# Kernel tuning notes

Hardware: AMD Instinct MI355X
Metric: run time of the kernel (lower is better)

## Reference

```python
import jax, jax.numpy as jnp
import numpy as np

N_NODES = 50000
N_EDGES = 800000
IN_FEAT = 128
INTER_DIM = 128
OUT_FEAT = 128
EDGE_W_DIM = 3


def setup_inputs() -> dict:
    key = jax.random.key(0)
    ks = jax.random.split(key, 8)
    h = jax.random.normal(ks[0], (N_NODES, IN_FEAT), dtype=jnp.float32)
    edge_src = jax.random.randint(ks[1], (N_EDGES,), 0, N_NODES, dtype=jnp.int32)
    edge_dst = jax.random.randint(ks[2], (N_EDGES,), 0, N_NODES, dtype=jnp.int32)
    edge_w = jax.random.normal(ks[3], (N_EDGES, EDGE_W_DIM), dtype=jnp.float32)
    # xavier-normal-ish init, gain for relu
    gain = float(np.sqrt(2.0))
    W1 = jax.random.normal(ks[4], (INTER_DIM, IN_FEAT + EDGE_W_DIM), dtype=jnp.float32)
    W1 = W1 * (gain * np.sqrt(2.0 / (INTER_DIM + IN_FEAT + EDGE_W_DIM)))
    b1 = jnp.zeros((INTER_DIM,), dtype=jnp.float32)
    W2 = jax.random.normal(ks[5], (OUT_FEAT, IN_FEAT + INTER_DIM), dtype=jnp.float32)
    W2 = W2 * (gain * np.sqrt(2.0 / (OUT_FEAT + IN_FEAT + INTER_DIM)))
    b2 = jnp.zeros((OUT_FEAT,), dtype=jnp.float32)
    return {"h": h, "edge_src": edge_src, "edge_dst": edge_dst, "edge_w": edge_w,
            "W1": W1, "b1": b1, "W2": W2, "b2": b2}


def reference(h, edge_src, edge_dst, edge_w, W1, b1, W2, b2):
    n_nodes = h.shape[0]
    # per-edge message: concat(src node feature, edge weight) -> [E, in_feat+3]
    m = jnp.concatenate([h[edge_src], edge_w], axis=1)
    # linear1 + leaky_relu (torch default negative_slope=0.01)
    tmp = m @ W1.T + b1  # [E, inter_dim]
    tmp = jnp.where(tmp >= 0, tmp, 0.01 * tmp)
    # mean over incoming edges per destination node; zero-in-degree nodes get 0
    sums = jax.ops.segment_sum(tmp, edge_dst, num_segments=n_nodes)
    counts = jax.ops.segment_sum(jnp.ones((tmp.shape[0],), dtype=tmp.dtype),
                                 edge_dst, num_segments=n_nodes)
    h_N = sums / jnp.maximum(counts, 1.0)[:, None]  # [N, inter_dim]
    # tail: concat + linear2 + relu
    h_total = jnp.concatenate([h, h_N], axis=1)  # [N, in_feat+inter_dim]
    return jax.nn.relu(h_total @ W2.T + b2)
```

## Files before the change

kernel.cpp:

```cpp
#include <hip/hip_runtime.h>
#include <hip/hip_bf16.h>

#define N_NODES 50000
#define N_EDGES 800000
#define N_TILES 3125
#define CSR_BLOCKS 782
#define PROJ_BLOCKS 782
#define BUCKET_CAP 64

typedef __attribute__((ext_vector_type(8))) short short8;
typedef __attribute__((ext_vector_type(4))) float f32x4;
typedef __attribute__((ext_vector_type(2))) float fl2;

#define OFF_G     0
#define OFF_CUR   1600000
#define OFF_HN    6400000
#define OFF_W1BP  12866384
#define OFF_BP1   12866896
#define OFF_BP2   12875088


__device__ inline unsigned bf16rne(float f) {
    unsigned u = __float_as_uint(f);
    return (u + 0x7fffu + ((u >> 16) & 1u)) >> 16;
}
__device__ inline unsigned pk2(float lo, float hi) {
    return bf16rne(lo) | (bf16rne(hi) << 16);
}
union FragU { unsigned u[4]; short8 s; uint4 v; };

template <bool HI>
__device__ inline fl2 fp8x2_dec_w(unsigned s) {
#if __has_builtin(__builtin_amdgcn_cvt_pk_f32_fp8)
    return __builtin_amdgcn_cvt_pk_f32_fp8((int)s, HI);
#else
    unsigned v = HI ? (s >> 16) : s;
    fl2 r;
    unsigned lo = v & 0xffu, h2 = (v >> 8) & 0xffu;
    unsigned blo = ((lo & 0x80u) << 24) | ((lo & 0x7fu) << 20);
    unsigned bhi = ((h2 & 0x80u) << 24) | ((h2 & 0x7fu) << 20);
    r.x = __uint_as_float(blo) * 0x1p120f;
    r.y = __uint_as_float(bhi) * 0x1p120f;
    return r;
#endif
}
__device__ inline unsigned fp8x4_enc(float a, float b, float c, float d) {
#if __has_builtin(__builtin_amdgcn_cvt_pk_fp8_f32)
    int u = __builtin_amdgcn_cvt_pk_fp8_f32(a, b, 0, false);
    u = __builtin_amdgcn_cvt_pk_fp8_f32(c, d, u, true);
    return (unsigned)u;
#else
    auto enc1 = [](float f) -> unsigned {
        unsigned u = __float_as_uint(f);
        unsigned sg = (u >> 24) & 0x80u;
        float af = fabsf(f);
        if (af < 0x1p-6f) return sg;
        if (af >= 448.f) return sg | 0x7eu;
        unsigned v = __float_as_uint(af);
        unsigned r = v + 0xFFFFFu + ((v >> 20) & 1u);
        unsigned E = r >> 23, m = (r >> 20) & 7u;
        return sg | ((E - 120u) << 3) | m;
    };
    return enc1(a) | (enc1(b) << 8) | (enc1(c) << 16) | (enc1(d) << 24);
#endif
}

__global__ __launch_bounds__(256) void repack_zero_kernel(
        const float* __restrict__ W1, const float* __restrict__ b1,
        const float* __restrict__ W2, float* __restrict__ W1bp,
        uint4* __restrict__ Bpack1, uint4* __restrict__ Bpack2,
        int* __restrict__ cursor) {
    int tid = blockIdx.x * 256 + threadIdx.x;
    if (tid < 2048) {
        int lane = tid & 63, ent = tid >> 6;
        int n = (ent & 7) * 16 + (lane & 15);
        int k0 = (ent >> 3) * 32 + ((lane >> 4) << 3);
        const float* src = W1 + n * 131 + k0;
        FragU f;
        f.u[0] = pk2(src[0], src[1]);
        f.u[1] = pk2(src[2], src[3]);
        f.u[2] = pk2(src[4], src[5]);
        f.u[3] = pk2(src[6], src[7]);
        Bpack1[ent * 64 + lane] = f.v;
    } else if (tid < 6144) {
        int t2 = tid - 2048;
        int lane = t2 & 63, ent = t2 >> 6;
        int n = (ent & 7) * 16 + (lane & 15);
        int k0 = (ent >> 3) * 32 + ((lane >> 4) << 3);
        const float* src = W2 + n * 256 + k0;
        FragU f;
        f.u[0] = pk2(src[0], src[1]);
        f.u[1] = pk2(src[2], src[3]);
        f.u[2] = pk2(src[4], src[5]);
        f.u[3] = pk2(src[6], src[7]);
        Bpack2[ent * 64 + lane] = f.v;
    }
    if (tid < 128) {
        W1bp[tid * 4 + 0] = W1[tid * 131 + 128];
        W1bp[tid * 4 + 1] = W1[tid * 131 + 129];
        W1bp[tid * 4 + 2] = W1[tid * 131 + 130];
        W1bp[tid * 4 + 3] = b1[tid];
    }
    if (tid < N_NODES) cursor[tid] = 0;
}

__global__ __launch_bounds__(256) void fused_bucket_proj(
        const int* __restrict__ esrc, const int* __restrict__ edst,
        const float* __restrict__ ew, int* __restrict__ cursor,
        uint2* __restrict__ bkt,
        const float* __restrict__ h, const uint4* __restrict__ Bpack1,
        unsigned* __restrict__ g8) {
    __shared__ float lds[64][132];
    const int role = blockIdx.x & 1;
    const int gb = blockIdx.x >> 1;

    if (role == 0) {
        const int base = gb * 1024 + threadIdx.x;
        int dst[4], src[4];
        float w0[4], w1[4], w2[4];
        bool ok[4];
        #pragma unroll
        for (int j = 0; j < 4; j++) {
            int e = base + j * 256;
            ok[j] = e < N_EDGES;
            int ce = ok[j] ? e : 0;
            dst[j] = edst[ce];
            src[j] = esrc[ce];
            w0[j] = ew[ce * 3 + 0];
            w1[j] = ew[ce * 3 + 1];
            w2[j] = ew[ce * 3 + 2];
        }
        int pos[4];
        #pragma unroll
        for (int j = 0; j < 4; j++)
            pos[j] = ok[j] ? atomicAdd(&cursor[dst[j]], 1) : BUCKET_CAP;
        #pragma unroll
        for (int j = 0; j < 4; j++) {
            if (ok[j] && pos[j] < BUCKET_CAP) {
                uint2 rec;
                rec.x = (unsigned)src[j] | (bf16rne(w0[j]) << 16);
                rec.y = bf16rne(w1[j]) | (bf16rne(w2[j]) << 16);
                bkt[(dst[j] << 6) + pos[j]] = rec;
            }
        }
        return;
    }

    const int wave = threadIdx.x >> 6;
    const int lane = threadIdx.x & 63;
    const int T = gb * 4 + wave;

    if (T < N_TILES) {
        f32x4 acc[8];
        #pragma unroll
        for (int i = 0; i < 8; i++) acc[i] = (f32x4)(0.f);

        const int row = T * 16 + (lane & 15);
        const float* hrow = h + row * 128 + ((lane >> 4) << 3);

        #pragma unroll
        for (int kt = 0; kt < 4; kt++) {
            float4 x0 = *(const float4*)(hrow + kt * 32);
            float4 x1 = *(const float4*)(hrow + kt * 32 + 4);
            FragU a;
            a.u[0] = pk2(x0.x, x0.y);
            a.u[1] = pk2(x0.z, x0.w);
            a.u[2] = pk2(x1.x, x1.y);
            a.u[3] = pk2(x1.z, x1.w);
            #pragma unroll
            for (int nt = 0; nt < 8; nt++) {
                FragU b;
                b.v = Bpack1[(kt * 8 + nt) * 64 + lane];
                acc[nt] = __builtin_amdgcn_mfma_f32_16x16x32_bf16(a.s, b.s, acc[nt], 0, 0, 0);
            }
        }
        #pragma unroll
        for (int nt = 0; nt < 8; nt++) {
            #pragma unroll
            for (int reg = 0; reg < 4; reg++) {
                int r = ((lane >> 4) << 2) + reg;
                lds[wave * 16 + r][nt * 16 + (lane & 15)] = acc[nt][reg];
            }
        }
    }
    __syncthreads();

    const int t = threadIdx.x;
    const int nodeL = t >> 2, seg = t & 3;
    const int gnode = gb * 64 + nodeL;
    if (gnode < N_NODES) {
        #pragma unroll
        for (int i = 0; i < 2; i++) {
            const float* p = &lds[nodeL][seg * 32 + i * 16];
            uint4 o;
            o.x = fp8x4_enc(p[0],  p[1],  p[2],  p[3]);
            o.y = fp8x4_enc(p[4],  p[5],  p[6],  p[7]);
            o.z = fp8x4_enc(p[8],  p[9],  p[10], p[11]);
            o.w = fp8x4_enc(p[12], p[13], p[14], p[15]);
            ((uint4*)g8)[gnode * 8 + seg * 2 + i] = o;
        }
    }
}

#define AGG_P 4
__global__ __launch_bounds__(256) void agg_kernel(const unsigned* __restrict__ g8u,
                                                  const uint2* __restrict__ bkt,
                                                  const int* __restrict__ cursor,
                                                  const float* __restrict__ W1bp,
                                                  float* __restrict__ hN) {
    const int wave = threadIdx.x >> 6;
    const int lane = threadIdx.x & 63;
    const int half = lane >> 5;
    const int c = lane & 31;
    const int v = blockIdx.x * 4 + wave;
    if (v >= N_NODES) return;

    const int degT = cursor[v];
    const int deg = (degT < BUCKET_CAP) ? degT : BUCKET_CAP;
    const int beg = v << 6;
    const int end = beg + deg;

    const float4 w0 = ((const float4*)W1bp)[4 * c + 0];
    const float4 w1 = ((const float4*)W1bp)[4 * c + 1];
    const float4 w2 = ((const float4*)W1bp)[4 * c + 2];
    const float4 w3 = ((const float4*)W1bp)[4 * c + 3];
    const fl2 cx0 = {w0.x, w1.x}, cx1 = {w2.x, w3.x};
    const fl2 cy0 = {w0.y, w1.y}, cy1 = {w2.y, w3.y};
    const fl2 cz0 = {w0.z, w1.z}, cz1 = {w2.z, w3.z};
    const fl2 cb0 = {w0.w, w1.w}, cb1 = {w2.w, w3.w};
    const fl2 kP = (fl2)(0.505f);
    const fl2 kA = (fl2)(0.495f);

    fl2 acc0 = (fl2)(0.f), acc1 = (fl2)(0.f);

    int i = beg;
    for (; i + 2 * AGG_P <= end; i += 2 * AGG_P) {
        uint2 r[AGG_P];
        #pragma unroll
        for (int u = 0; u < AGG_P; u++) r[u] = bkt[i + 2 * u + half];
        unsigned gv[AGG_P];
        #pragma unroll
        for (int u = 0; u < AGG_P; u++) gv[u] = g8u[(r[u].x & 0xffffu) * 32 + c];
        #pragma unroll
        for (int u = 0; u < AGG_P; u++) {
            fl2 ry = (fl2)(__uint_as_float(r[u].x & 0xffff0000u));
            fl2 rz = (fl2)(__uint_as_float(r[u].y << 16));
            fl2 rw = (fl2)(__uint_as_float(r[u].y & 0xffff0000u));
            fl2 t0 = fp8x2_dec_w<false>(gv[u]) + cb0;
            t0 = __builtin_elementwise_fma(cx0, ry, t0);
            t0 = __builtin_elementwise_fma(cy0, rz, t0);
            t0 = __builtin_elementwise_fma(cz0, rw, t0);
            acc0 = __builtin_elementwise_fma(kP, t0, acc0);
            acc0 = __builtin_elementwise_fma(kA, __builtin_elementwise_abs(t0), acc0);
            fl2 t1 = fp8x2_dec_w<true>(gv[u]) + cb1;
            t1 = __builtin_elementwise_fma(cx1, ry, t1);
            t1 = __builtin_elementwise_fma(cy1, rz, t1);
            t1 = __builtin_elementwise_fma(cz1, rw, t1);
            acc1 = __builtin_elementwise_fma(kP, t1, acc1);
            acc1 = __builtin_elementwise_fma(kA, __builtin_elementwise_abs(t1), acc1);
        }
    }
    for (; i + 2 <= end; i += 2) {
        uint2 r = bkt[i + half];
        unsigned gv = g8u[(r.x & 0xffffu) * 32 + c];
        fl2 ry = (fl2)(__uint_as_float(r.x & 0xffff0000u));
        fl2 rz = (fl2)(__uint_as_float(r.y << 16));
        fl2 rw = (fl2)(__uint_as_float(r.y & 0xffff0000u));
        fl2 t0 = fp8x2_dec_w<false>(gv) + cb0;
        t0 = __builtin_elementwise_fma(cx0, ry, t0);
        t0 = __builtin_elementwise_fma(cy0, rz, t0);
        t0 = __builtin_elementwise_fma(cz0, rw, t0);
        acc0 = __builtin_elementwise_fma(kP, t0, acc0);
        acc0 = __builtin_elementwise_fma(kA, __builtin_elementwise_abs(t0), acc0);
        fl2 t1 = fp8x2_dec_w<true>(gv) + cb1;
        t1 = __builtin_elementwise_fma(cx1, ry, t1);
        t1 = __builtin_elementwise_fma(cy1, rz, t1);
        t1 = __builtin_elementwise_fma(cz1, rw, t1);
        acc1 = __builtin_elementwise_fma(kP, t1, acc1);
        acc1 = __builtin_elementwise_fma(kA, __builtin_elementwise_abs(t1), acc1);
    }
    if (i < end) {
        float sc = (half == 0) ? 1.f : 0.f;
        fl2 sP = (fl2)(0.505f * sc), sA = (fl2)(0.495f * sc);
        uint2 r = bkt[i];
        unsigned gv = g8u[(r.x & 0xffffu) * 32 + c];
        fl2 ry = (fl2)(__uint_as_float(r.x & 0xffff0000u));
        fl2 rz = (fl2)(__uint_as_float(r.y << 16));
        fl2 rw = (fl2)(__uint_as_float(r.y & 0xffff0000u));
        fl2 t0 = fp8x2_dec_w<false>(gv) + cb0;
        t0 = __builtin_elementwise_fma(cx0, ry, t0);
        t0 = __builtin_elementwise_fma(cy0, rz, t0);
        t0 = __builtin_elementwise_fma(cz0, rw, t0);
        acc0 = __builtin_elementwise_fma(sP, t0, acc0);
        acc0 = __builtin_elementwise_fma(sA, __builtin_elementwise_abs(t0), acc0);
        fl2 t1 = fp8x2_dec_w<true>(gv) + cb1;
        t1 = __builtin_elementwise_fma(cx1, ry, t1);
        t1 = __builtin_elementwise_fma(cy1, rz, t1);
        t1 = __builtin_elementwise_fma(cz1, rw, t1);
        acc1 = __builtin_elementwise_fma(sP, t1, acc1);
        acc1 = __builtin_elementwise_fma(sA, __builtin_elementwise_abs(t1), acc1);
    }

    acc0.x += __shfl_xor(acc0.x, 32);
    acc0.y += __shfl_xor(acc0.y, 32);
    acc1.x += __shfl_xor(acc1.x, 32);
    acc1.y += __shfl_xor(acc1.y, 32);
    if (half == 0) {
        float inv = 1.0f / (float)((degT > 0) ? degT : 1);
        float4 o;
        o.x = acc0.x * inv;
        o.y = acc0.y * inv;
        o.z = acc1.x * inv;
        o.w = acc1.y * inv;
        ((float4*)hN)[v * 32 + c] = o;
    }
}

__global__ __launch_bounds__(256) void final_mfma(const float* __restrict__ h,
                                                  const float* __restrict__ hN,
                                                  const uint4* __restrict__ Bpack2,
                                                  const float* __restrict__ b2,
                                                  float* __restrict__ out) {
    const int wave = threadIdx.x >> 6;
    const int lane = threadIdx.x & 63;
    const int T = blockIdx.x * 4 + wave;
    if (T >= N_TILES) return;

    f32x4 acc[8];
    #pragma unroll
    for (int i = 0; i < 8; i++) acc[i] = (f32x4)(0.f);

    const int row = T * 16 + (lane & 15);
    const int koff = (lane >> 4) << 3;
    const float* hrow = h + row * 128 + koff;
    const float* nrow = hN + row * 128 + koff;

    #pragma unroll
    for (int kt = 0; kt < 8; kt++) {
        const float* src = (kt < 4) ? (hrow + kt * 32) : (nrow + (kt - 4) * 32);
        float4 x0 = *(const float4*)(src);
        float4 x1 = *(const float4*)(src + 4);
        FragU a;
        a.u[0] = pk2(x0.x, x0.y);
        a.u[1] = pk2(x0.z, x0.w);
        a.u[2] = pk2(x1.x, x1.y);
        a.u[3] = pk2(x1.z, x1.w);
        #pragma unroll
        for (int nt = 0; nt < 8; nt++) {
            FragU b;
            b.v = Bpack2[(kt * 8 + nt) * 64 + lane];
            acc[nt] = __builtin_amdgcn_mfma_f32_16x16x32_bf16(a.s, b.s, acc[nt], 0, 0, 0);
        }
    }
    #pragma unroll
    for (int nt = 0; nt < 8; nt++) {
        int ch = nt * 16 + (lane & 15);
        float bias = b2[ch];
        #pragma unroll
        for (int reg = 0; reg < 4; reg++) {
            int node = T * 16 + ((lane >> 4) << 2) + reg;
            out[node * 128 + ch] = fmaxf(acc[nt][reg] + bias, 0.f);
        }
    }
}

extern "C" void kernel_launch(void* const* d_in, const int* in_sizes, int n_in,
                              void* d_out, int out_size, void* d_ws, size_t ws_size,
                              hipStream_t stream) {
    const float* h    = (const float*)d_in[0];
    const int*   esrc = (const int*)d_in[1];
    const int*   edst = (const int*)d_in[2];
    const float* ew   = (const float*)d_in[3];
    const float* W1   = (const float*)d_in[4];
    const float* b1   = (const float*)d_in[5];
    const float* W2   = (const float*)d_in[6];
    const float* b2   = (const float*)d_in[7];
    float* out = (float*)d_out;
    float* ws  = (float*)d_ws;

    unsigned* g8  = (unsigned*)(ws + OFF_G);
    int* cursor   = (int*)(ws + OFF_CUR);
    float* hN     = ws + OFF_HN;
    float* W1bp   = ws + OFF_W1BP;
    uint4* Bpack1 = (uint4*)(ws + OFF_BP1);
    uint4* Bpack2 = (uint4*)(ws + OFF_BP2);

    uint2* bkt = (uint2*)d_out;

    repack_zero_kernel<<<196, 256, 0, stream>>>(W1, b1, W2, W1bp, Bpack1, Bpack2, cursor);

    fused_bucket_proj<<<CSR_BLOCKS + PROJ_BLOCKS, 256, 0, stream>>>(
        esrc, edst, ew, cursor, bkt, h, Bpack1, g8);

    agg_kernel<<<(N_NODES + 3) / 4, 256, 0, stream>>>(g8, bkt, cursor, W1bp, hN);

    final_mfma<<<(N_TILES + 3) / 4, 256, 0, stream>>>(h, hN, Bpack2, b2, out);
}
```

Baseline: 197.9 us.

## Fuse neighbor aggregation into final MFMA kernel via per-wave LDS tile

Merges the aggregation kernel and the final linear2 MFMA kernel. Each wave now aggregates 16 consecutive nodes sequentially and stores the resulting h_N rows as bf16 in a swizzled LDS tile, which is then read directly as MFMA A-fragments. This removes the fp32 h_N round trip through global memory and one kernel launch. The bucket array moves from the output buffer into workspace. The cost is far less parallelism for the gather phase: 782 blocks each walking 16 nodes serially per wave, instead of one node per wave over 12500 blocks, which may leave memory latency less hidden.

```diff
diff --git a/kernel.cpp b/kernel.cpp
--- a/kernel.cpp
+++ b/kernel.cpp
@@ -6,6 +6,7 @@
 #define N_TILES 3125
 #define CSR_BLOCKS 782
 #define PROJ_BLOCKS 782
+#define AF_BLOCKS 782
 #define BUCKET_CAP 64
 
 typedef __attribute__((ext_vector_type(8))) short short8;
@@ -14,11 +15,10 @@
 
 #define OFF_G     0
 #define OFF_CUR   1600000
-#define OFF_HN    6400000
+#define OFF_BKT   6400000
 #define OFF_W1BP  12866384
 #define OFF_BP1   12866896
 #define OFF_BP2   12875088
-
 
 __device__ inline unsigned bf16rne(float f) {
     unsigned u = __float_as_uint(f);
@@ -203,22 +203,19 @@
 }
 
 #define AGG_P 4
-__global__ __launch_bounds__(256) void agg_kernel(const unsigned* __restrict__ g8u,
-                                                  const uint2* __restrict__ bkt,
-                                                  const int* __restrict__ cursor,
-                                                  const float* __restrict__ W1bp,
-                                                  float* __restrict__ hN) {
+__global__ __launch_bounds__(256) void agg_final(
+        const unsigned* __restrict__ g8u, const uint2* __restrict__ bkt,
+        const int* __restrict__ cursor, const float* __restrict__ W1bp,
+        const float* __restrict__ h, const uint4* __restrict__ Bpack2,
+        const float* __restrict__ b2, float* __restrict__ out) {
+    __shared__ __align__(16) unsigned ldsN[4][16 * 64];
     const int wave = threadIdx.x >> 6;
     const int lane = threadIdx.x & 63;
     const int half = lane >> 5;
     const int c = lane & 31;
-    const int v = blockIdx.x * 4 + wave;
-    if (v >= N_NODES) return;
-
-    const int degT = cursor[v];
-    const int deg = (degT < BUCKET_CAP) ? degT : BUCKET_CAP;
-    const int beg = v << 6;
-    const int end = beg + deg;
+    int T = blockIdx.x * 4 + wave;
+    const bool live = (T < N_TILES);
+    if (!live) T = 0;
 
     const float4 w0 = ((const float4*)W1bp)[4 * c + 0];
     const float4 w1 = ((const float4*)W1bp)[4 * c + 1];
@@ -231,100 +228,74 @@
     const fl2 kP = (fl2)(0.505f);
     const fl2 kA = (fl2)(0.495f);
 
-    fl2 acc0 = (fl2)(0.f), acc1 = (fl2)(0.f);
-
-    int i = beg;
-    for (; i + 2 * AGG_P <= end; i += 2 * AGG_P) {
-        uint2 r[AGG_P];
-        #pragma unroll
-        for (int u = 0; u < AGG_P; u++) r[u] = bkt[i + 2 * u + half];
-        unsigned gv[AGG_P];
-        #pragma unroll
-        for (int u = 0; u < AGG_P; u++) gv[u] = g8u[(r[u].x & 0xffffu) * 32 + c];
-        #pragma unroll
-        for (int u = 0; u < AGG_P; u++) {
-            fl2 ry = (fl2)(__uint_as_float(r[u].x & 0xffff0000u));
-            fl2 rz = (fl2)(__uint_as_float(r[u].y << 16));
-            fl2 rw = (fl2)(__uint_as_float(r[u].y & 0xffff0000u));
-            fl2 t0 = fp8x2_dec_w<false>(gv[u]) + cb0;
-            t0 = __builtin_elementwise_fma(cx0, ry, t0);
-            t0 = __builtin_elementwise_fma(cy0, rz, t0);
-            t0 = __builtin_elementwise_fma(cz0, rw, t0);
-            acc0 = __builtin_elementwise_fma(kP, t0, acc0);
-            acc0 = __builtin_elementwise_fma(kA, __builtin_elementwise_abs(t0), acc0);
-            fl2 t1 = fp8x2_dec_w<true>(gv[u]) + cb1;
-            t1 = __builtin_elementwise_fma(cx1, ry, t1);
-            t1 = __builtin_elementwise_fma(cy1, rz, t1);
-            t1 = __builtin_elementwise_fma(cz1, rw, t1);
-            acc1 = __builtin_elementwise_fma(kP, t1, acc1);
-            acc1 = __builtin_elementwise_fma(kA, __builtin_elementwise_abs(t1), acc1);
-        }
-    }
-    for (; i + 2 <= end; i += 2) {
-        uint2 r = bkt[i + half];
-        unsigned gv = g8u[(r.x & 0xffffu) * 32 + c];
-        fl2 ry = (fl2)(__uint_as_float(r.x & 0xffff0000u));
-        fl2 rz = (fl2)(__uint_as_float(r.y << 16));
-        fl2 rw = (fl2)(__uint_as_float(r.y & 0xffff0000u));
-        fl2 t0 = fp8x2_dec_w<false>(gv) + cb0;
-        t0 = __builtin_elementwise_fma(cx0, ry, t0);
-        t0 = __builtin_elementwise_fma(cy0, rz, t0);
-        t0 = __builtin_elementwise_fma(cz0, rw, t0);
-        acc0 = __builtin_elementwise_fma(kP, t0, acc0);
-        acc0 = __builtin_elementwise_fma(kA, __builtin_elementwise_abs(t0), acc0);
-        fl2 t1 = fp8x2_dec_w<true>(gv) + cb1;
-        t1 = __builtin_elementwise_fma(cx1, ry, t1);
-        t1 = __builtin_elementwise_fma(cy1, rz, t1);
-        t1 = __builtin_elementwise_fma(cz1, rw, t1);
-        acc1 = __builtin_elementwise_fma(kP, t1, acc1);
-        acc1 = __builtin_elementwise_fma(kA, __builtin_elementwise_abs(t1), acc1);
-    }
-    if (i < end) {
-        float sc = (half == 0) ? 1.f : 0.f;
-        fl2 sP = (fl2)(0.505f * sc), sA = (fl2)(0.495f * sc);
-        uint2 r = bkt[i];
-        unsigned gv = g8u[(r.x & 0xffffu) * 32 + c];
-        fl2 ry = (fl2)(__uint_as_float(r.x & 0xffff0000u));
-        fl2 rz = (fl2)(__uint_as_float(r.y << 16));
-        fl2 rw = (fl2)(__uint_as_float(r.y & 0xffff0000u));
-        fl2 t0 = fp8x2_dec_w<false>(gv) + cb0;
-        t0 = __builtin_elementwise_fma(cx0, ry, t0);
-        t0 = __builtin_elementwise_fma(cy0, rz, t0);
-        t0 = __builtin_elementwise_fma(cz0, rw, t0);
-        acc0 = __builtin_elementwise_fma(sP, t0, acc0);
-        acc0 = __builtin_elementwise_fma(sA, __builtin_elementwise_abs(t0), acc0);
-        fl2 t1 = fp8x2_dec_w<true>(gv) + cb1;
-        t1 = __builtin_elementwise_fma(cx1, ry, t1);
-        t1 = __builtin_elementwise_fma(cy1, rz, t1);
-        t1 = __builtin_elementwise_fma(cz1, rw, t1);
-        acc1 = __builtin_elementwise_fma(sP, t1, acc1);
-        acc1 = __builtin_elementwise_fma(sA, __builtin_elementwise_abs(t1), acc1);
-    }
-
-    acc0.x += __shfl_xor(acc0.x, 32);
-    acc0.y += __shfl_xor(acc0.y, 32);
-    acc1.x += __shfl_xor(acc1.x, 32);
-    acc1.y += __shfl_xor(acc1.y, 32);
-    if (half == 0) {
-        float inv = 1.0f / (float)((degT > 0) ? degT : 1);
-        float4 o;
-        o.x = acc0.x * inv;
-        o.y = acc0.y * inv;
-        o.z = acc1.x * inv;
-        o.w = acc1.y * inv;
-        ((float4*)hN)[v * 32 + c] = o;
-    }
-}
-
-__global__ __launch_bounds__(256) void final_mfma(const float* __restrict__ h,
-                                                  const float* __restrict__ hN,
-                                                  const uint4* __restrict__ Bpack2,
-                                                  const float* __restrict__ b2,
-                                                  float* __restrict__ out) {
-    const int wave = threadIdx.x >> 6;
-    const int lane = threadIdx.x & 63;
-    const int T = blockIdx.x * 4 + wave;
-    if (T >= N_TILES) return;
+    unsigned* myl = ldsN[wave];
+
+#define EDGE_BODY(R, GV, SP, SA)                                                       \
+    do {                                                                               \
+        fl2 ry = (fl2)(__uint_as_float((R).x & 0xffff0000u));                          \
+        fl2 rz = (fl2)(__uint_as_float((R).y << 16));                                  \
+        fl2 rw = (fl2)(__uint_as_float((R).y & 0xffff0000u));                          \
+        fl2 t0 = fp8x2_dec_w<false>(GV) + cb0;                                         \
+        t0 = __builtin_elementwise_fma(cx0, ry, t0);                                   \
+        t0 = __builtin_elementwise_fma(cy0, rz, t0);                                   \
+        t0 = __builtin_elementwise_fma(cz0, rw, t0);                                   \
+        acc0 = __builtin_elementwise_fma(SP, t0, acc0);                                \
+        acc0 = __builtin_elementwise_fma(SA, __builtin_elementwise_abs(t0), acc0);     \
+        fl2 t1 = fp8x2_dec_w<true>(GV) + cb1;                                          \
+        t1 = __builtin_elementwise_fma(cx1, ry, t1);                                   \
+        t1 = __builtin_elementwise_fma(cy1, rz, t1);                                   \
+        t1 = __builtin_elementwise_fma(cz1, rw, t1);                                   \
+        acc1 = __builtin_elementwise_fma(SP, t1, acc1);                                \
+        acc1 = __builtin_elementwise_fma(SA, __builtin_elementwise_abs(t1), acc1);     \
+    } while (0)
+
+    for (int n = 0; n < 16; n++) {
+        const int v = T * 16 + n;
+        const int degT = cursor[v];
+        const int deg = (degT < BUCKET_CAP) ? degT : BUCKET_CAP;
+        const int beg = v << 6;
+        const int end = beg + deg;
+        fl2 acc0 = (fl2)(0.f), acc1 = (fl2)(0.f);
+
+        int i = beg;
+        for (; i + 2 * AGG_P <= end; i += 2 * AGG_P) {
+            uint2 r[AGG_P];
+            #pragma unroll
+            for (int u = 0; u < AGG_P; u++) r[u] = bkt[i + 2 * u + half];
+            unsigned gv[AGG_P];
+            #pragma unroll
+            for (int u = 0; u < AGG_P; u++) gv[u] = g8u[(r[u].x & 0xffffu) * 32 + c];
+            #pragma unroll
+            for (int u = 0; u < AGG_P; u++) EDGE_BODY(r[u], gv[u], kP, kA);
+        }
+        for (; i + 2 <= end; i += 2) {
+            uint2 r = bkt[i + half];
+            unsigned gv = g8u[(r.x & 0xffffu) * 32 + c];
+            EDGE_BODY(r, gv, kP, kA);
+        }
+        if (i < end) {
+            float sc = (half == 0) ? 1.f : 0.f;
+            fl2 sP = (fl2)(0.505f * sc), sA = (fl2)(0.495f * sc);
+            uint2 r = bkt[i];
+            unsigned gv = g8u[(r.x & 0xffffu) * 32 + c];
+            EDGE_BODY(r, gv, sP, sA);
+        }
+
+        acc0.x += __shfl_xor(acc0.x, 32);
+        acc0.y += __shfl_xor(acc0.y, 32);
+        acc1.x += __shfl_xor(acc1.x, 32);
+        acc1.y += __shfl_xor(acc1.y, 32);
+        if (half == 0) {
+            float inv = 1.0f / (float)((degT > 0) ? degT : 1);
+            uint2 p;
+            p.x = pk2(acc0.x * inv, acc0.y * inv);
+            p.y = pk2(acc1.x * inv, acc1.y * inv);
+            const int idx = (2 * c) ^ ((n & 7) << 2);
+            *(uint2*)&myl[n * 64 + idx] = p;
+        }
+    }
+#undef EDGE_BODY
+    __syncthreads();
 
     f32x4 acc[8];
     #pragma unroll
@@ -333,18 +304,22 @@
     const int row = T * 16 + (lane & 15);
     const int koff = (lane >> 4) << 3;
     const float* hrow = h + row * 128 + koff;
-    const float* nrow = hN + row * 128 + koff;
 
     #pragma unroll
     for (int kt = 0; kt < 8; kt++) {
-        const float* src = (kt < 4) ? (hrow + kt * 32) : (nrow + (kt - 4) * 32);
-        float4 x0 = *(const float4*)(src);
-        float4 x1 = *(const float4*)(src + 4);
         FragU a;
-        a.u[0] = pk2(x0.x, x0.y);
-        a.u[1] = pk2(x0.z, x0.w);
-        a.u[2] = pk2(x1.x, x1.y);
-        a.u[3] = pk2(x1.z, x1.w);
+        if (kt < 4) {
+            float4 x0 = *(const float4*)(hrow + kt * 32);
+            float4 x1 = *(const float4*)(hrow + kt * 32 + 4);
+            a.u[0] = pk2(x0.x, x0.y);
+            a.u[1] = pk2(x0.z, x0.w);
+            a.u[2] = pk2(x1.x, x1.y);
+            a.u[3] = pk2(x1.z, x1.w);
+        } else {
+            const int nn = lane & 15;
+            const int idx = (((kt - 4) << 4) + (koff >> 1)) ^ ((nn & 7) << 2);
+            a.v = *(const uint4*)&myl[nn * 64 + idx];
+        }
         #pragma unroll
         for (int nt = 0; nt < 8; nt++) {
             FragU b;
@@ -352,14 +327,16 @@
             acc[nt] = __builtin_amdgcn_mfma_f32_16x16x32_bf16(a.s, b.s, acc[nt], 0, 0, 0);
         }
     }
-    #pragma unroll
-    for (int nt = 0; nt < 8; nt++) {
-        int ch = nt * 16 + (lane & 15);
-        float bias = b2[ch];
-        #pragma unroll
-        for (int reg = 0; reg < 4; reg++) {
-            int node = T * 16 + ((lane >> 4) << 2) + reg;
-            out[node * 128 + ch] = fmaxf(acc[nt][reg] + bias, 0.f);
+    if (live) {
+        #pragma unroll
+        for (int nt = 0; nt < 8; nt++) {
+            int ch = nt * 16 + (lane & 15);
+            float bias = b2[ch];
+            #pragma unroll
+            for (int reg = 0; reg < 4; reg++) {
+                int node = T * 16 + ((lane >> 4) << 2) + reg;
+                out[node * 128 + ch] = fmaxf(acc[nt][reg] + bias, 0.f);
+            }
         }
     }
 }
@@ -380,19 +357,15 @@
 
     unsigned* g8  = (unsigned*)(ws + OFF_G);
     int* cursor   = (int*)(ws + OFF_CUR);
-    float* hN     = ws + OFF_HN;
     float* W1bp   = ws + OFF_W1BP;
     uint4* Bpack1 = (uint4*)(ws + OFF_BP1);
     uint4* Bpack2 = (uint4*)(ws + OFF_BP2);
-
-    uint2* bkt = (uint2*)d_out;
+    uint2* bkt    = (uint2*)(ws + OFF_BKT);
 
     repack_zero_kernel<<<196, 256, 0, stream>>>(W1, b1, W2, W1bp, Bpack1, Bpack2, cursor);
 
     fused_bucket_proj<<<CSR_BLOCKS + PROJ_BLOCKS, 256, 0, stream>>>(
         esrc, edst, ew, cursor, bkt, h, Bpack1, g8);
 
-    agg_kernel<<<(N_NODES + 3) / 4, 256, 0, stream>>>(g8, bkt, cursor, W1bp, hN);
-
-    final_mfma<<<(N_TILES + 3) / 4, 256, 0, stream>>>(h, hN, Bpack2, b2, out);
-}
+    agg_final<<<AF_BLOCKS, 256, 0, stream>>>(g8, bkt, cursor, W1bp, h, Bpack2, b2, out);
+}
```

Result: no change. 199.0 us (+0.5%).
